# Kernel tuning notes

Measured on AMD Instinct MI355X. Metric: run time of the kernel, lower is better.

## Reference

```python
import jax, jax.numpy as jnp
import numpy as np

DEGREE = 8
HIDDEN = 256
IN_DIM = 3
N_LAYERS = 8  # num_hidden_layers=8 -> 1 input + 6 middle + 1 output ChebyKAN layers


def cheby_layer(x, coeff):
    """x: [P, in], coeff: [in, out, degree+1] -> [P, out].
    Computes tanh(x), Chebyshev recurrence T_0..T_d, and contracts
    sum_d T_d(x)_i * coeff[i, o, d] without materializing the full basis.
    """
    x = jnp.tanh(x)
    t_prev = jnp.ones_like(x)          # T_0
    t_cur = x                          # T_1
    out = jnp.einsum('pi,io->po', t_prev, coeff[:, :, 0])
    out = out + jnp.einsum('pi,io->po', t_cur, coeff[:, :, 1])
    for d in range(2, coeff.shape[-1]):
        t_prev, t_cur = t_cur, 2.0 * x * t_cur - t_prev
        out = out + jnp.einsum('pi,io->po', t_cur, coeff[:, :, d])
    return out


def decode(pts, ws):
    h = pts
    for w in ws:
        h = cheby_layer(h, w)
    return h


def setup_inputs() -> dict:
    key = jax.random.key(0)
    k_nm, k_m, *k_ws = jax.random.split(key, 2 + N_LAYERS)
    B, N = 4, 16384
    inp = {
        'non_mnfld_pnts': jax.random.normal(k_nm, (B, N, IN_DIM), dtype=jnp.float32),
        'mnfld_pnts': jax.random.normal(k_m, (B, N, IN_DIM), dtype=jnp.float32),
    }
    dims = [IN_DIM] + [HIDDEN] * (N_LAYERS - 1) + [1]
    for i in range(N_LAYERS):
        fan_in, fan_out = dims[i], dims[i + 1]
        std = 1.0 / (fan_in * (DEGREE + 1))
        inp[f'w{i}'] = jax.random.normal(k_ws[i], (fan_in, fan_out, DEGREE + 1), dtype=jnp.float32) * std
    return inp


def reference(non_mnfld_pnts, mnfld_pnts, w0, w1, w2, w3, w4, w5, w6, w7):
    ws = [w0, w1, w2, w3, w4, w5, w6, w7]
    B = non_mnfld_pnts.shape[0]
    mnfld_pred = decode(mnfld_pnts.reshape(-1, IN_DIM), ws).reshape(B, -1)
    nonmnfld_pred = decode(non_mnfld_pnts.reshape(-1, IN_DIM), ws).reshape(B, -1)
    return (mnfld_pred, nonmnfld_pred)
```

## Files before the change

### kernel.cpp

```cpp
#include <hip/hip_runtime.h>

typedef _Float16 f16;
typedef __attribute__((ext_vector_type(4)))  _Float16 f16x4;
typedef __attribute__((ext_vector_type(8)))  _Float16 f16x8;
typedef __attribute__((ext_vector_type(16))) float    f32x16;

#define WT_L (8*256*256)

__device__ __forceinline__ float fexp2(float x) {
#if __has_builtin(__builtin_amdgcn_exp2f)
    return __builtin_amdgcn_exp2f(x);
#else
    return exp2f(x);
#endif
}

__device__ __forceinline__ float fast_tanh(float v) {
    float a = __builtin_fabsf(v);
    float e = fexp2(a * -2.8853900817779268f);
    float r = (1.0f - e) * __builtin_amdgcn_rcpf(1.0f + e);
    return __builtin_copysignf(r, v);
}

__global__ void prep_mid(const float* __restrict__ w, f16* __restrict__ wt, float* __restrict__ biasL) {
    __shared__ float red[256];
    const int i = threadIdx.x;
    const int o = blockIdx.x;
    float v[9];
#pragma unroll
    for (int d = 0; d < 9; d++) v[d] = w[(i*256 + o)*9 + d];
#pragma unroll
    for (int d = 1; d < 9; d++) wt[((d-1)*256 + o)*256 + i] = (f16)v[d];
    red[i] = v[0];
    __syncthreads();
#pragma unroll
    for (int s = 128; s > 0; s >>= 1) {
        if (i < s) red[i] += red[i + s];
        __syncthreads();
    }
    if (i == 0) biasL[o] = red[0];
}

__global__ void prep_w0(const float* __restrict__ w0, float* __restrict__ w0t) {
    int id = blockIdx.x*256 + threadIdx.x;
    int i = id / 2304, rem = id % 2304;
    int o = rem / 9, d = rem % 9;
    w0t[(i*9 + d)*256 + o] = w0[id];
}

__global__ void prep_w7(const float* __restrict__ w7, float* __restrict__ w7p) {
    int id = blockIdx.x*256 + threadIdx.x;
    int ch = id / 9, d = id % 9;
    w7p[ch*12 + d] = w7[id];
}

__global__ __launch_bounds__(256, 2)
void kan_mfma(const float* __restrict__ nonm, const float* __restrict__ mnf,
              const f16* __restrict__ wt, const float* __restrict__ bias,
              const float* __restrict__ w0t, const float* __restrict__ w7p,
              float* __restrict__ out)
{
    __shared__ __align__(16) f16 xs[128*256];

    const int t    = threadIdx.x;
    const int b    = blockIdx.x;
    const int lane = t & 63;
    const int w    = t >> 6;
    const int l31  = lane & 31;
    const int half = lane >> 5;
    const int nb   = w * 64;

    const float* src = (b < 512) ? mnf : nonm;
    const int p0 = ((b < 512) ? b : (b - 512)) * 128;

    {
        const int pt = t >> 1;
        const int oh = (t & 1) * 128;
        float c0 = src[(p0 + pt)*3 + 0];
        float c1 = src[(p0 + pt)*3 + 1];
        float c2 = src[(p0 + pt)*3 + 2];
        float xx[3] = {fast_tanh(c0), fast_tanh(c1), fast_tanh(c2)};
        float bas[27];
#pragma unroll
        for (int i = 0; i < 3; i++) {
            float t0 = 1.0f, t1 = xx[i];
            bas[i*9+0] = t0; bas[i*9+1] = t1;
            float x2 = xx[i] + xx[i];
#pragma unroll
            for (int d = 2; d < 9; d++) {
                float t2 = x2*t1 - t0;
                bas[i*9+d] = t2; t0 = t1; t1 = t2;
            }
        }
#pragma unroll 1
        for (int q = 0; q < 32; q++) {
            int o = oh + q*4;
            float4 a = {0.f, 0.f, 0.f, 0.f};
#pragma unroll
            for (int k = 0; k < 27; k++) {
                float4 wv = *(const float4*)(w0t + k*256 + o);
                a.x = fmaf(bas[k], wv.x, a.x);
                a.y = fmaf(bas[k], wv.y, a.y);
                a.z = fmaf(bas[k], wv.z, a.z);
                a.w = fmaf(bas[k], wv.w, a.w);
            }
            f16x4 hv = {(f16)fast_tanh(a.x), (f16)fast_tanh(a.y),
                        (f16)fast_tanh(a.z), (f16)fast_tanh(a.w)};
            int unit = (o >> 3) ^ (pt & 7);
            *(f16x4*)(xs + pt*256 + unit*8 + (o & 7)) = hv;
        }
    }
    __syncthreads();

    f32x16 acc[4][2];
    const f16x8 ones = {(f16)1.f,(f16)1.f,(f16)1.f,(f16)1.f,(f16)1.f,(f16)1.f,(f16)1.f,(f16)1.f};

#pragma unroll 1
    for (int L = 0; L < 6; L++) {
        const f16* wbase = wt + L*WT_L + half*8 + (nb + l31)*256;
        float b0 = bias[L*256 + nb + l31];
        float b1 = bias[L*256 + nb + 32 + l31];
#pragma unroll
        for (int mt = 0; mt < 4; mt++)
#pragma unroll
            for (int r = 0; r < 16; r++) { acc[mt][0][r] = b0; acc[mt][1][r] = b1; }

        f16x8 xv[4], Bb[4][2];
#pragma unroll
        for (int mt = 0; mt < 4; mt++) {
            int m = mt*32 + l31;
            int unit = half ^ (m & 7);
            xv[mt] = *(const f16x8*)(xs + m*256 + unit*8);
        }
#pragma unroll
        for (int j = 0; j < 4; j++) {
            Bb[j][0] = *(const f16x8*)(wbase + j*65536);
            Bb[j][1] = *(const f16x8*)(wbase + j*65536 + 8192);
        }

        f16x8 x2[4], t1[4], t0[4];
#pragma unroll 1
        for (int ck = 0; ck < 16; ck++) {
            const int ckn = (ck < 15) ? ck + 1 : 15;
#pragma unroll
            for (int mt = 0; mt < 4; mt++) {
                t1[mt] = xv[mt];
                x2[mt] = xv[mt] + xv[mt];
                t0[mt] = ones;
            }
#pragma unroll
            for (int mt = 0; mt < 4; mt++) {
                int m = mt*32 + l31;
                int unit = (ckn*2 + half) ^ (m & 7);
                xv[mt] = *(const f16x8*)(xs + m*256 + unit*8);
            }
#pragma unroll
            for (int j = 0; j < 8; j++) {
                const int ck2 = (j < 4) ? ck : ckn;
                const int j2  = (j < 4) ? (j + 4) : (j - 4);
                f16x8 nb0 = *(const f16x8*)(wbase + ck2*16 + j2*65536);
                f16x8 nb1 = *(const f16x8*)(wbase + ck2*16 + j2*65536 + 8192);
#pragma unroll
                for (int mt = 0; mt < 4; mt++) {
                    acc[mt][0] = __builtin_amdgcn_mfma_f32_32x32x16_f16(t1[mt], Bb[j&3][0], acc[mt][0], 0, 0, 0);
                    acc[mt][1] = __builtin_amdgcn_mfma_f32_32x32x16_f16(t1[mt], Bb[j&3][1], acc[mt][1], 0, 0, 0);
                }
                if (j < 7) {
#pragma unroll
                    for (int mt = 0; mt < 4; mt++) {
                        f16x8 tn = x2[mt]*t1[mt] - t0[mt];
                        t0[mt] = t1[mt];
                        t1[mt] = tn;
                    }
                }
                Bb[j&3][0] = nb0;
                Bb[j&3][1] = nb1;
            }
        }
        __syncthreads();
#pragma unroll
        for (int mt = 0; mt < 4; mt++) {
#pragma unroll
            for (int nt = 0; nt < 2; nt++) {
                int ch = nb + nt*32 + l31;
                int cu = ch >> 3, ce = ch & 7;
#pragma unroll
                for (int r = 0; r < 16; r++) {
                    int p = mt*32 + (r & 3) + 8*(r >> 2) + 4*half;
                    int unit = cu ^ (p & 7);
                    xs[p*256 + unit*8 + ce] = (f16)fast_tanh(acc[mt][nt][r]);
                }
            }
        }
        __syncthreads();
    }

    {
        const int pt = t & 127;
        const int hh = t >> 7;
        float s = 0.0f;
#pragma unroll 1
        for (int q = 0; q < 16; q++) {
            int u = hh*16 + q;
            int unit = u ^ (pt & 7);
            f16x8 xv = *(const f16x8*)(xs + pt*256 + unit*8);
#pragma unroll
            for (int e = 0; e < 8; e++) {
                int ch = u*8 + e;
                float x = (float)xv[e];
                const float* wr = w7p + ch*12;
                float4 wa = *(const float4*)(wr);
                float4 wb = *(const float4*)(wr + 4);
                float wc = wr[8];
                float x2 = x + x;
                float t0 = 1.0f, t1v = x;
                s = fmaf(wa.x, t0, s);
                s = fmaf(wa.y, t1v, s);
                float t2 = x2*t1v - t0;  s = fmaf(wa.z, t2, s);
                float t3 = x2*t2 - t1v;  s = fmaf(wa.w, t3, s);
                float t4 = x2*t3 - t2;   s = fmaf(wb.x, t4, s);
                float t5 = x2*t4 - t3;   s = fmaf(wb.y, t5, s);
                float t6 = x2*t5 - t4;   s = fmaf(wb.z, t6, s);
                float t7 = x2*t6 - t5;   s = fmaf(wb.w, t7, s);
                float t8 = x2*t7 - t6;   s = fmaf(wc,  t8, s);
            }
        }
        __syncthreads();
        float* red = (float*)xs;
        red[hh*128 + pt] = s;
        __syncthreads();
        if (t < 128) out[b*128 + t] = red[t] + red[128 + t];
    }
}

extern "C" void kernel_launch(void* const* d_in, const int* in_sizes, int n_in,
                              void* d_out, int out_size, void* d_ws, size_t ws_size,
                              hipStream_t stream) {
    const float* nonm = (const float*)d_in[0];
    const float* mnf  = (const float*)d_in[1];

    char* ws = (char*)d_ws;
    f16*   wtp   = (f16*)ws;
    float* biasp = (float*)(ws + 6*WT_L*2);
    float* w0tp  = (float*)(ws + 6*WT_L*2 + 6*256*4);
    float* w7pp  = (float*)(ws + 6*WT_L*2 + 6*256*4 + 27*256*4);

    for (int L = 0; L < 6; L++)
        prep_mid<<<256, 256, 0, stream>>>((const float*)d_in[3 + L], wtp + L*WT_L, biasp + L*256);
    prep_w0<<<27, 256, 0, stream>>>((const float*)d_in[2], w0tp);
    prep_w7<<<9, 256, 0, stream>>>((const float*)d_in[9], w7pp);

    kan_mfma<<<1024, 256, 0, stream>>>(nonm, mnf, wtp, biasp, w0tp, w7pp, (float*)d_out);
}
```

Baseline: 1.251 ms.

## Split fused KAN kernel into per-layer launches with global activation buffer

The single fused kernel that ran all eight layers per 128-point tile is split into separate kernels: an input-layer kernel, one MFMA kernel launch per middle layer, and an output-layer kernel. Activations round-trip through a global f16 buffer between launches. The first and last layers get their own thread mappings, and the output kernel stages its weights in shared memory. The intent is to improve occupancy and scheduling for the light first and last layers, at the cost of extra global traffic of about 64 MB per layer and several more kernel launches.

```diff
diff --git a/kernel.cpp b/kernel.cpp
--- a/kernel.cpp
+++ b/kernel.cpp
@@ -54,11 +54,51 @@
     w7p[ch*12 + d] = w7[id];
 }
 
+__global__ void k0(const float* __restrict__ nonm, const float* __restrict__ mnf,
+                   const float* __restrict__ w0t, f16* __restrict__ xg) {
+    const int t = threadIdx.x, b = blockIdx.x;
+    const int pt = t & 63;
+    const int oh = (t >> 6) * 64;
+    const int pid = b*64 + pt;
+    const float* src = (pid < 65536) ? mnf : nonm;
+    const int sp = (pid < 65536) ? pid : pid - 65536;
+    float c0 = src[sp*3 + 0];
+    float c1 = src[sp*3 + 1];
+    float c2 = src[sp*3 + 2];
+    float xx[3] = {fast_tanh(c0), fast_tanh(c1), fast_tanh(c2)};
+    float bas[27];
+#pragma unroll
+    for (int i = 0; i < 3; i++) {
+        float t0 = 1.0f, t1 = xx[i];
+        bas[i*9+0] = t0; bas[i*9+1] = t1;
+        float x2 = xx[i] + xx[i];
+#pragma unroll
+        for (int d = 2; d < 9; d++) {
+            float t2 = x2*t1 - t0;
+            bas[i*9+d] = t2; t0 = t1; t1 = t2;
+        }
+    }
+#pragma unroll 1
+    for (int q = 0; q < 16; q++) {
+        int o = oh + q*4;
+        float4 a = {0.f, 0.f, 0.f, 0.f};
+#pragma unroll
+        for (int k = 0; k < 27; k++) {
+            float4 wv = *(const float4*)(w0t + k*256 + o);
+            a.x = fmaf(bas[k], wv.x, a.x);
+            a.y = fmaf(bas[k], wv.y, a.y);
+            a.z = fmaf(bas[k], wv.z, a.z);
+            a.w = fmaf(bas[k], wv.w, a.w);
+        }
+        f16x4 hv = {(f16)fast_tanh(a.x), (f16)fast_tanh(a.y),
+                    (f16)fast_tanh(a.z), (f16)fast_tanh(a.w)};
+        *(f16x4*)(xg + (size_t)pid*256 + o) = hv;
+    }
+}
+
 __global__ __launch_bounds__(256, 2)
-void kan_mfma(const float* __restrict__ nonm, const float* __restrict__ mnf,
-              const f16* __restrict__ wt, const float* __restrict__ bias,
-              const float* __restrict__ w0t, const float* __restrict__ w7p,
-              float* __restrict__ out)
+void k_mid(const f16* __restrict__ wl, const float* __restrict__ biasL,
+           f16* __restrict__ xg)
 {
     __shared__ __align__(16) f16 xs[128*256];
 
@@ -69,168 +109,139 @@
     const int l31  = lane & 31;
     const int half = lane >> 5;
     const int nb   = w * 64;
-
-    const float* src = (b < 512) ? mnf : nonm;
-    const int p0 = ((b < 512) ? b : (b - 512)) * 128;
-
-    {
-        const int pt = t >> 1;
-        const int oh = (t & 1) * 128;
-        float c0 = src[(p0 + pt)*3 + 0];
-        float c1 = src[(p0 + pt)*3 + 1];
-        float c2 = src[(p0 + pt)*3 + 2];
-        float xx[3] = {fast_tanh(c0), fast_tanh(c1), fast_tanh(c2)};
-        float bas[27];
-#pragma unroll
-        for (int i = 0; i < 3; i++) {
-            float t0 = 1.0f, t1 = xx[i];
-            bas[i*9+0] = t0; bas[i*9+1] = t1;
-            float x2 = xx[i] + xx[i];
-#pragma unroll
-            for (int d = 2; d < 9; d++) {
-                float t2 = x2*t1 - t0;
-                bas[i*9+d] = t2; t0 = t1; t1 = t2;
-            }
-        }
-#pragma unroll 1
-        for (int q = 0; q < 32; q++) {
-            int o = oh + q*4;
-            float4 a = {0.f, 0.f, 0.f, 0.f};
-#pragma unroll
-            for (int k = 0; k < 27; k++) {
-                float4 wv = *(const float4*)(w0t + k*256 + o);
-                a.x = fmaf(bas[k], wv.x, a.x);
-                a.y = fmaf(bas[k], wv.y, a.y);
-                a.z = fmaf(bas[k], wv.z, a.z);
-                a.w = fmaf(bas[k], wv.w, a.w);
-            }
-            f16x4 hv = {(f16)fast_tanh(a.x), (f16)fast_tanh(a.y),
-                        (f16)fast_tanh(a.z), (f16)fast_tanh(a.w)};
-            int unit = (o >> 3) ^ (pt & 7);
-            *(f16x4*)(xs + pt*256 + unit*8 + (o & 7)) = hv;
-        }
+    const size_t tile_off = (size_t)b * 128 * 256;
+
+#pragma unroll
+    for (int i = 0; i < 16; i++) {
+        int idx = i*256 + t;
+        int pt = idx >> 5, cu = idx & 31;
+        f16x8 v = *(const f16x8*)(xg + tile_off + (size_t)idx*8);
+        *(f16x8*)(xs + pt*256 + ((cu ^ (pt & 7))*8)) = v;
     }
     __syncthreads();
 
     f32x16 acc[4][2];
     const f16x8 ones = {(f16)1.f,(f16)1.f,(f16)1.f,(f16)1.f,(f16)1.f,(f16)1.f,(f16)1.f,(f16)1.f};
 
+    const f16* wbase = wl + half*8 + (nb + l31)*256;
+    float b0 = biasL[nb + l31];
+    float b1 = biasL[nb + 32 + l31];
+#pragma unroll
+    for (int mt = 0; mt < 4; mt++)
+#pragma unroll
+        for (int r = 0; r < 16; r++) { acc[mt][0][r] = b0; acc[mt][1][r] = b1; }
+
+    f16x8 xv[4], Bb[4][2];
+#pragma unroll
+    for (int mt = 0; mt < 4; mt++) {
+        int m = mt*32 + l31;
+        int unit = half ^ (m & 7);
+        xv[mt] = *(const f16x8*)(xs + m*256 + unit*8);
+    }
+#pragma unroll
+    for (int j = 0; j < 4; j++) {
+        Bb[j][0] = *(const f16x8*)(wbase + j*65536);
+        Bb[j][1] = *(const f16x8*)(wbase + j*65536 + 8192);
+    }
+
+    f16x8 x2[4], t1[4], t0[4];
 #pragma unroll 1
-    for (int L = 0; L < 6; L++) {
-        const f16* wbase = wt + L*WT_L + half*8 + (nb + l31)*256;
-        float b0 = bias[L*256 + nb + l31];
-        float b1 = bias[L*256 + nb + 32 + l31];
-#pragma unroll
-        for (int mt = 0; mt < 4; mt++)
-#pragma unroll
-            for (int r = 0; r < 16; r++) { acc[mt][0][r] = b0; acc[mt][1][r] = b1; }
-
-        f16x8 xv[4], Bb[4][2];
+    for (int ck = 0; ck < 16; ck++) {
+        const int ckn = (ck < 15) ? ck + 1 : 15;
+#pragma unroll
+        for (int mt = 0; mt < 4; mt++) {
+            t1[mt] = xv[mt];
+            x2[mt] = xv[mt] + xv[mt];
+            t0[mt] = ones;
+        }
 #pragma unroll
         for (int mt = 0; mt < 4; mt++) {
             int m = mt*32 + l31;
-            int unit = half ^ (m & 7);
+            int unit = (ckn*2 + half) ^ (m & 7);
             xv[mt] = *(const f16x8*)(xs + m*256 + unit*8);
         }
 #pragma unroll
-        for (int j = 0; j < 4; j++) {
-            Bb[j][0] = *(const f16x8*)(wbase + j*65536);
-            Bb[j][1] = *(const f16x8*)(wbase + j*65536 + 8192);
-        }
-
-        f16x8 x2[4], t1[4], t0[4];
-#pragma unroll 1
-        for (int ck = 0; ck < 16; ck++) {
-            const int ckn = (ck < 15) ? ck + 1 : 15;
+        for (int j = 0; j < 8; j++) {
+            const int ck2 = (j < 4) ? ck : ckn;
+            const int j2  = (j < 4) ? (j + 4) : (j - 4);
+            f16x8 pb0 = *(const f16x8*)(wbase + ck2*16 + j2*65536);
+            f16x8 pb1 = *(const f16x8*)(wbase + ck2*16 + j2*65536 + 8192);
 #pragma unroll
             for (int mt = 0; mt < 4; mt++) {
-                t1[mt] = xv[mt];
-                x2[mt] = xv[mt] + xv[mt];
-                t0[mt] = ones;
+                acc[mt][0] = __builtin_amdgcn_mfma_f32_32x32x16_f16(t1[mt], Bb[j&3][0], acc[mt][0], 0, 0, 0);
+                acc[mt][1] = __builtin_amdgcn_mfma_f32_32x32x16_f16(t1[mt], Bb[j&3][1], acc[mt][1], 0, 0, 0);
             }
-#pragma unroll
-            for (int mt = 0; mt < 4; mt++) {
-                int m = mt*32 + l31;
-                int unit = (ckn*2 + half) ^ (m & 7);
-                xv[mt] = *(const f16x8*)(xs + m*256 + unit*8);
-            }
-#pragma unroll
-            for (int j = 0; j < 8; j++) {
-                const int ck2 = (j < 4) ? ck : ckn;
-                const int j2  = (j < 4) ? (j + 4) : (j - 4);
-                f16x8 nb0 = *(const f16x8*)(wbase + ck2*16 + j2*65536);
-                f16x8 nb1 = *(const f16x8*)(wbase + ck2*16 + j2*65536 + 8192);
+            if (j < 7) {
 #pragma unroll
                 for (int mt = 0; mt < 4; mt++) {
-                    acc[mt][0] = __builtin_amdgcn_mfma_f32_32x32x16_f16(t1[mt], Bb[j&3][0], acc[mt][0], 0, 0, 0);
-                    acc[mt][1] = __builtin_amdgcn_mfma_f32_32x32x16_f16(t1[mt], Bb[j&3][1], acc[mt][1], 0, 0, 0);
-                }
-                if (j < 7) {
-#pragma unroll
-                    for (int mt = 0; mt < 4; mt++) {
-                        f16x8 tn = x2[mt]*t1[mt] - t0[mt];
-                        t0[mt] = t1[mt];
-                        t1[mt] = tn;
-                    }
-                }
-                Bb[j&3][0] = nb0;
-                Bb[j&3][1] = nb1;
-            }
-        }
-        __syncthreads();
-#pragma unroll
-        for (int mt = 0; mt < 4; mt++) {
-#pragma unroll
-            for (int nt = 0; nt < 2; nt++) {
-                int ch = nb + nt*32 + l31;
-                int cu = ch >> 3, ce = ch & 7;
-#pragma unroll
-                for (int r = 0; r < 16; r++) {
-                    int p = mt*32 + (r & 3) + 8*(r >> 2) + 4*half;
-                    int unit = cu ^ (p & 7);
-                    xs[p*256 + unit*8 + ce] = (f16)fast_tanh(acc[mt][nt][r]);
+                    f16x8 tn = x2[mt]*t1[mt] - t0[mt];
+                    t0[mt] = t1[mt];
+                    t1[mt] = tn;
                 }
             }
-        }
-        __syncthreads();
-    }
-
-    {
-        const int pt = t & 127;
-        const int hh = t >> 7;
-        float s = 0.0f;
+            Bb[j&3][0] = pb0;
+            Bb[j&3][1] = pb1;
+        }
+    }
+    __syncthreads();
+
+#pragma unroll
+    for (int mt = 0; mt < 4; mt++) {
+#pragma unroll
+        for (int nt = 0; nt < 2; nt++) {
+            int ch = nb + nt*32 + l31;
+            int cu = ch >> 3, ce = ch & 7;
+#pragma unroll
+            for (int r = 0; r < 16; r++) {
+                int p = mt*32 + (r & 3) + 8*(r >> 2) + 4*half;
+                int unit = cu ^ (p & 7);
+                xs[p*256 + unit*8 + ce] = (f16)fast_tanh(acc[mt][nt][r]);
+            }
+        }
+    }
+    __syncthreads();
+
+#pragma unroll
+    for (int i = 0; i < 16; i++) {
+        int idx = i*256 + t;
+        int pt = idx >> 5, cu = idx & 31;
+        f16x8 v = *(const f16x8*)(xs + pt*256 + ((cu ^ (pt & 7))*8));
+        *(f16x8*)(xg + tile_off + (size_t)idx*8) = v;
+    }
+}
+
+__global__ void k7(const f16* __restrict__ xg, const float* __restrict__ w7p,
+                   float* __restrict__ out) {
+    __shared__ float w7s[256*12];
+    const int t = threadIdx.x, b = blockIdx.x;
+#pragma unroll
+    for (int i = 0; i < 12; i++) w7s[i*256 + t] = w7p[i*256 + t];
+    __syncthreads();
+    const int pid = b*256 + t;
+    const f16* row = xg + (size_t)pid*256;
+    float s = 0.0f;
 #pragma unroll 1
-        for (int q = 0; q < 16; q++) {
-            int u = hh*16 + q;
-            int unit = u ^ (pt & 7);
-            f16x8 xv = *(const f16x8*)(xs + pt*256 + unit*8);
-#pragma unroll
-            for (int e = 0; e < 8; e++) {
-                int ch = u*8 + e;
-                float x = (float)xv[e];
-                const float* wr = w7p + ch*12;
-                float4 wa = *(const float4*)(wr);
-                float4 wb = *(const float4*)(wr + 4);
-                float wc = wr[8];
-                float x2 = x + x;
-                float t0 = 1.0f, t1v = x;
-                s = fmaf(wa.x, t0, s);
-                s = fmaf(wa.y, t1v, s);
-                float t2 = x2*t1v - t0;  s = fmaf(wa.z, t2, s);
-                float t3 = x2*t2 - t1v;  s = fmaf(wa.w, t3, s);
-                float t4 = x2*t3 - t2;   s = fmaf(wb.x, t4, s);
-                float t5 = x2*t4 - t3;   s = fmaf(wb.y, t5, s);
-                float t6 = x2*t5 - t4;   s = fmaf(wb.z, t6, s);
-                float t7 = x2*t6 - t5;   s = fmaf(wb.w, t7, s);
-                float t8 = x2*t7 - t6;   s = fmaf(wc,  t8, s);
-            }
-        }
-        __syncthreads();
-        float* red = (float*)xs;
-        red[hh*128 + pt] = s;
-        __syncthreads();
-        if (t < 128) out[b*128 + t] = red[t] + red[128 + t];
-    }
+    for (int cu = 0; cu < 32; cu++) {
+        f16x8 xv = *(const f16x8*)(row + cu*8);
+#pragma unroll
+        for (int e = 0; e < 8; e++) {
+            int ch = cu*8 + e;
+            const float* wr = w7s + ch*12;
+            float x = (float)xv[e];
+            float x2 = x + x;
+            float t0 = 1.0f, t1v = x;
+            s = fmaf(wr[0], t0, s);
+            s = fmaf(wr[1], t1v, s);
+            float t2 = x2*t1v - t0;  s = fmaf(wr[2], t2, s);
+            float t3 = x2*t2 - t1v;  s = fmaf(wr[3], t3, s);
+            float t4 = x2*t3 - t2;   s = fmaf(wr[4], t4, s);
+            float t5 = x2*t4 - t3;   s = fmaf(wr[5], t5, s);
+            float t6 = x2*t5 - t4;   s = fmaf(wr[6], t6, s);
+            float t7 = x2*t6 - t5;   s = fmaf(wr[7], t7, s);
+            float t8 = x2*t7 - t6;   s = fmaf(wr[8], t8, s);
+        }
+    }
+    out[pid] = s;
 }
 
 extern "C" void kernel_launch(void* const* d_in, const int* in_sizes, int n_in,
@@ -242,13 +253,17 @@
     char* ws = (char*)d_ws;
     f16*   wtp   = (f16*)ws;
     float* biasp = (float*)(ws + 6*WT_L*2);
-    float* w0tp  = (float*)(ws + 6*WT_L*2 + 6*256*4);
-    float* w7pp  = (float*)(ws + 6*WT_L*2 + 6*256*4 + 27*256*4);
+    float* w0tp  = (float*)(ws + 6*WT_L*2 + 6144);
+    float* w7pp  = (float*)(ws + 6*WT_L*2 + 6144 + 27648);
+    f16*   xg    = (f16*)(ws + 6*WT_L*2 + 6144 + 27648 + 12288);
 
     for (int L = 0; L < 6; L++)
         prep_mid<<<256, 256, 0, stream>>>((const float*)d_in[3 + L], wtp + L*WT_L, biasp + L*256);
     prep_w0<<<27, 256, 0, stream>>>((const float*)d_in[2], w0tp);
     prep_w7<<<9, 256, 0, stream>>>((const float*)d_in[9], w7pp);
 
-    kan_mfma<<<1024, 256, 0, stream>>>(nonm, mnf, wtp, biasp, w0tp, w7pp, (float*)d_out);
-}
+    k0<<<2048, 256, 0, stream>>>(nonm, mnf, w0tp, xg);
+    for (int L = 0; L < 6; L++)
+        k_mid<<<1024, 256, 0, stream>>>(wtp + L*WT_L, biasp + L*256, xg);
+    k7<<<512, 256, 0, stream>>>(xg, w7pp, (float*)d_out);
+}
```

Result: no change. 1.233 ms (-1.4%).

## Merge weight prep kernels and split fused MLP into three staged kernels

Applied to the files above, without the earlier changes.

Folds the eight weight-preparation launches into one prep_all kernel. Splits the single persistent kernel into three kernels, each running two layers, that pass activations through a global fp16 scratch buffer. This likely aims to cut launch overhead and to shorten each kernel, perhaps for better scheduling or code generation. In exchange it adds global round-trips for the 128x256 activation tiles and two extra kernel boundaries.

```diff
diff --git a/kernel.cpp b/kernel.cpp
--- a/kernel.cpp
+++ b/kernel.cpp
@@ -22,63 +22,176 @@
     return __builtin_copysignf(r, v);
 }
 
-__global__ void prep_mid(const float* __restrict__ w, f16* __restrict__ wt, float* __restrict__ biasL) {
+__global__ void prep_all(const float* __restrict__ w0, const float* __restrict__ w1,
+                         const float* __restrict__ w2, const float* __restrict__ w3,
+                         const float* __restrict__ w4, const float* __restrict__ w5,
+                         const float* __restrict__ w6, const float* __restrict__ w7,
+                         f16* __restrict__ wt, float* __restrict__ biasp,
+                         float* __restrict__ w0t, float* __restrict__ w7p)
+{
     __shared__ float red[256];
-    const int i = threadIdx.x;
-    const int o = blockIdx.x;
-    float v[9];
-#pragma unroll
-    for (int d = 0; d < 9; d++) v[d] = w[(i*256 + o)*9 + d];
-#pragma unroll
-    for (int d = 1; d < 9; d++) wt[((d-1)*256 + o)*256 + i] = (f16)v[d];
-    red[i] = v[0];
+    const int bi = blockIdx.x, t = threadIdx.x;
+    if (bi < 1536) {
+        const int L = bi >> 8, o = bi & 255, i = t;
+        const float* w;
+        switch (L) { case 0: w = w1; break; case 1: w = w2; break; case 2: w = w3; break;
+                     case 3: w = w4; break; case 4: w = w5; break; default: w = w6; }
+        float v[9];
+#pragma unroll
+        for (int d = 0; d < 9; d++) v[d] = w[(i*256 + o)*9 + d];
+#pragma unroll
+        for (int d = 1; d < 9; d++) wt[L*WT_L + ((d-1)*256 + o)*256 + i] = (f16)v[d];
+        red[i] = v[0];
+        __syncthreads();
+#pragma unroll
+        for (int s = 128; s > 0; s >>= 1) {
+            if (i < s) red[i] += red[i + s];
+            __syncthreads();
+        }
+        if (i == 0) biasp[L*256 + o] = red[0];
+    } else if (bi < 1563) {
+        int id = (bi - 1536)*256 + t;
+        int i = id / 2304, rem = id % 2304;
+        int o = rem / 9, d = rem % 9;
+        w0t[(i*9 + d)*256 + o] = w0[id];
+    } else {
+        int id = (bi - 1563)*256 + t;
+        int ch = id / 9, d = id % 9;
+        w7p[ch*12 + d] = w7[id];
+    }
+}
+
+__device__ __forceinline__ void gemm_layer(f16* __restrict__ xs,
+                                           const f16* __restrict__ wl,
+                                           const float* __restrict__ biasL,
+                                           int l31, int half, int nb)
+{
+    f32x16 acc[4][2];
+    const f16x8 ones = {(f16)1.f,(f16)1.f,(f16)1.f,(f16)1.f,(f16)1.f,(f16)1.f,(f16)1.f,(f16)1.f};
+
+    const f16* wbase = wl + half*8 + (nb + l31)*256;
+    float b0 = biasL[nb + l31];
+    float b1 = biasL[nb + 32 + l31];
+#pragma unroll
+    for (int mt = 0; mt < 4; mt++)
+#pragma unroll
+        for (int r = 0; r < 16; r++) { acc[mt][0][r] = b0; acc[mt][1][r] = b1; }
+
+    f16x8 xv[4], Bb[4][2];
+#pragma unroll
+    for (int mt = 0; mt < 4; mt++) {
+        int m = mt*32 + l31;
+        int unit = half ^ (m & 7);
+        xv[mt] = *(const f16x8*)(xs + m*256 + unit*8);
+    }
+#pragma unroll
+    for (int j = 0; j < 4; j++) {
+        Bb[j][0] = *(const f16x8*)(wbase + j*65536);
+        Bb[j][1] = *(const f16x8*)(wbase + j*65536 + 8192);
+    }
+
+    f16x8 x2[4], t1[4], t0[4];
+#pragma unroll 1
+    for (int ck = 0; ck < 16; ck++) {
+        const int ckn = (ck < 15) ? ck + 1 : 15;
+#pragma unroll
+        for (int mt = 0; mt < 4; mt++) {
+            t1[mt] = xv[mt];
+            x2[mt] = xv[mt] + xv[mt];
+            t0[mt] = ones;
+        }
+#pragma unroll
+        for (int mt = 0; mt < 4; mt++) {
+            int m = mt*32 + l31;
+            int unit = (ckn*2 + half) ^ (m & 7);
+            xv[mt] = *(const f16x8*)(xs + m*256 + unit*8);
+        }
+#pragma unroll
+        for (int j = 0; j < 8; j++) {
+            const int ck2 = (j < 4) ? ck : ckn;
+            const int j2  = (j < 4) ? (j + 4) : (j - 4);
+            f16x8 pb0 = *(const f16x8*)(wbase + ck2*16 + j2*65536);
+            f16x8 pb1 = *(const f16x8*)(wbase + ck2*16 + j2*65536 + 8192);
+#pragma unroll
+            for (int mt = 0; mt < 4; mt++) {
+                acc[mt][0] = __builtin_amdgcn_mfma_f32_32x32x16_f16(t1[mt], Bb[j&3][0], acc[mt][0], 0, 0, 0);
+                acc[mt][1] = __builtin_amdgcn_mfma_f32_32x32x16_f16(t1[mt], Bb[j&3][1], acc[mt][1], 0, 0, 0);
+            }
+            if (j < 7) {
+#pragma unroll
+                for (int mt = 0; mt < 4; mt++) {
+                    f16x8 tn = x2[mt]*t1[mt] - t0[mt];
+                    t0[mt] = t1[mt];
+                    t1[mt] = tn;
+                }
+            }
+            Bb[j&3][0] = pb0;
+            Bb[j&3][1] = pb1;
+        }
+    }
     __syncthreads();
-#pragma unroll
-    for (int s = 128; s > 0; s >>= 1) {
-        if (i < s) red[i] += red[i + s];
-        __syncthreads();
-    }
-    if (i == 0) biasL[o] = red[0];
-}
-
-__global__ void prep_w0(const float* __restrict__ w0, float* __restrict__ w0t) {
-    int id = blockIdx.x*256 + threadIdx.x;
-    int i = id / 2304, rem = id % 2304;
-    int o = rem / 9, d = rem % 9;
-    w0t[(i*9 + d)*256 + o] = w0[id];
-}
-
-__global__ void prep_w7(const float* __restrict__ w7, float* __restrict__ w7p) {
-    int id = blockIdx.x*256 + threadIdx.x;
-    int ch = id / 9, d = id % 9;
-    w7p[ch*12 + d] = w7[id];
+
+#pragma unroll
+    for (int mt = 0; mt < 4; mt++) {
+#pragma unroll
+        for (int nt = 0; nt < 2; nt++) {
+            int ch = nb + nt*32 + l31;
+            int cu = ch >> 3, ce = ch & 7;
+#pragma unroll
+            for (int r = 0; r < 16; r++) {
+                int p = mt*32 + (r & 3) + 8*(r >> 2) + 4*half;
+                int unit = cu ^ (p & 7);
+                xs[p*256 + unit*8 + ce] = (f16)fast_tanh(acc[mt][nt][r]);
+            }
+        }
+    }
+    __syncthreads();
+}
+
+__device__ __forceinline__ void stage_in(f16* __restrict__ xs, const f16* __restrict__ xg,
+                                         size_t tile_off, int t)
+{
+#pragma unroll
+    for (int i = 0; i < 16; i++) {
+        int idx = i*256 + t;
+        int cu = idx >> 7, pt = idx & 127;
+        f16x8 v = *(const f16x8*)(xg + tile_off + (size_t)idx*8);
+        *(f16x8*)(xs + pt*256 + ((cu ^ (pt & 7))*8)) = v;
+    }
+    __syncthreads();
+}
+
+__device__ __forceinline__ void stage_out(const f16* __restrict__ xs, f16* __restrict__ xg,
+                                          size_t tile_off, int t)
+{
+#pragma unroll
+    for (int i = 0; i < 16; i++) {
+        int idx = i*256 + t;
+        int cu = idx >> 7, pt = idx & 127;
+        f16x8 v = *(const f16x8*)(xs + pt*256 + ((cu ^ (pt & 7))*8));
+        *(f16x8*)(xg + tile_off + (size_t)idx*8) = v;
+    }
 }
 
 __global__ __launch_bounds__(256, 2)
-void kan_mfma(const float* __restrict__ nonm, const float* __restrict__ mnf,
-              const f16* __restrict__ wt, const float* __restrict__ bias,
-              const float* __restrict__ w0t, const float* __restrict__ w7p,
-              float* __restrict__ out)
+void kA(const float* __restrict__ nonm, const float* __restrict__ mnf,
+        const float* __restrict__ w0t, const f16* __restrict__ wt,
+        const float* __restrict__ bias, f16* __restrict__ xg)
 {
     __shared__ __align__(16) f16 xs[128*256];
-
-    const int t    = threadIdx.x;
-    const int b    = blockIdx.x;
-    const int lane = t & 63;
-    const int w    = t >> 6;
-    const int l31  = lane & 31;
-    const int half = lane >> 5;
-    const int nb   = w * 64;
-
-    const float* src = (b < 512) ? mnf : nonm;
-    const int p0 = ((b < 512) ? b : (b - 512)) * 128;
+    const int t = threadIdx.x, b = blockIdx.x;
+    const int lane = t & 63, w = t >> 6;
+    const int l31 = lane & 31, half = lane >> 5, nb = w * 64;
 
     {
         const int pt = t >> 1;
         const int oh = (t & 1) * 128;
-        float c0 = src[(p0 + pt)*3 + 0];
-        float c1 = src[(p0 + pt)*3 + 1];
-        float c2 = src[(p0 + pt)*3 + 2];
+        const int pid = b*128 + pt;
+        const float* src = (pid < 65536) ? mnf : nonm;
+        const int sp = (pid < 65536) ? pid : pid - 65536;
+        float c0 = src[sp*3 + 0];
+        float c1 = src[sp*3 + 1];
+        float c2 = src[sp*3 + 2];
         float xx[3] = {fast_tanh(c0), fast_tanh(c1), fast_tanh(c2)};
         float bas[27];
 #pragma unroll
@@ -112,103 +225,55 @@
     }
     __syncthreads();
 
-    f32x16 acc[4][2];
-    const f16x8 ones = {(f16)1.f,(f16)1.f,(f16)1.f,(f16)1.f,(f16)1.f,(f16)1.f,(f16)1.f,(f16)1.f};
-
-#pragma unroll 1
-    for (int L = 0; L < 6; L++) {
-        const f16* wbase = wt + L*WT_L + half*8 + (nb + l31)*256;
-        float b0 = bias[L*256 + nb + l31];
-        float b1 = bias[L*256 + nb + 32 + l31];
-#pragma unroll
-        for (int mt = 0; mt < 4; mt++)
-#pragma unroll
-            for (int r = 0; r < 16; r++) { acc[mt][0][r] = b0; acc[mt][1][r] = b1; }
-
-        f16x8 xv[4], Bb[4][2];
-#pragma unroll
-        for (int mt = 0; mt < 4; mt++) {
-            int m = mt*32 + l31;
-            int unit = half ^ (m & 7);
-            xv[mt] = *(const f16x8*)(xs + m*256 + unit*8);
-        }
-#pragma unroll
-        for (int j = 0; j < 4; j++) {
-            Bb[j][0] = *(const f16x8*)(wbase + j*65536);
-            Bb[j][1] = *(const f16x8*)(wbase + j*65536 + 8192);
-        }
-
-        f16x8 x2[4], t1[4], t0[4];
-#pragma unroll 1
-        for (int ck = 0; ck < 16; ck++) {
-            const int ckn = (ck < 15) ? ck + 1 : 15;
-#pragma unroll
-            for (int mt = 0; mt < 4; mt++) {
-                t1[mt] = xv[mt];
-                x2[mt] = xv[mt] + xv[mt];
-                t0[mt] = ones;
-            }
-#pragma unroll
-            for (int mt = 0; mt < 4; mt++) {
-                int m = mt*32 + l31;
-                int unit = (ckn*2 + half) ^ (m & 7);
-                xv[mt] = *(const f16x8*)(xs + m*256 + unit*8);
-            }
-#pragma unroll
-            for (int j = 0; j < 8; j++) {
-                const int ck2 = (j < 4) ? ck : ckn;
-                const int j2  = (j < 4) ? (j + 4) : (j - 4);
-                f16x8 nb0 = *(const f16x8*)(wbase + ck2*16 + j2*65536);
-                f16x8 nb1 = *(const f16x8*)(wbase + ck2*16 + j2*65536 + 8192);
-#pragma unroll
-                for (int mt = 0; mt < 4; mt++) {
-                    acc[mt][0] = __builtin_amdgcn_mfma_f32_32x32x16_f16(t1[mt], Bb[j&3][0], acc[mt][0], 0, 0, 0);
-                    acc[mt][1] = __builtin_amdgcn_mfma_f32_32x32x16_f16(t1[mt], Bb[j&3][1], acc[mt][1], 0, 0, 0);
-                }
-                if (j < 7) {
-#pragma unroll
-                    for (int mt = 0; mt < 4; mt++) {
-                        f16x8 tn = x2[mt]*t1[mt] - t0[mt];
-                        t0[mt] = t1[mt];
-                        t1[mt] = tn;
-                    }
-                }
-                Bb[j&3][0] = nb0;
-                Bb[j&3][1] = nb1;
-            }
-        }
-        __syncthreads();
-#pragma unroll
-        for (int mt = 0; mt < 4; mt++) {
-#pragma unroll
-            for (int nt = 0; nt < 2; nt++) {
-                int ch = nb + nt*32 + l31;
-                int cu = ch >> 3, ce = ch & 7;
-#pragma unroll
-                for (int r = 0; r < 16; r++) {
-                    int p = mt*32 + (r & 3) + 8*(r >> 2) + 4*half;
-                    int unit = cu ^ (p & 7);
-                    xs[p*256 + unit*8 + ce] = (f16)fast_tanh(acc[mt][nt][r]);
-                }
-            }
-        }
-        __syncthreads();
-    }
+    gemm_layer(xs, wt + 0*WT_L, bias + 0*256, l31, half, nb);
+    gemm_layer(xs, wt + 1*WT_L, bias + 1*256, l31, half, nb);
+
+    stage_out(xs, xg, (size_t)b * 32768, t);
+}
+
+__global__ __launch_bounds__(256, 2)
+void kB(const f16* __restrict__ wt, const float* __restrict__ bias, f16* __restrict__ xg)
+{
+    __shared__ __align__(16) f16 xs[128*256];
+    const int t = threadIdx.x, b = blockIdx.x;
+    const int lane = t & 63, w = t >> 6;
+    const int l31 = lane & 31, half = lane >> 5, nb = w * 64;
+    const size_t tile_off = (size_t)b * 32768;
+
+    stage_in(xs, xg, tile_off, t);
+    gemm_layer(xs, wt + 2*WT_L, bias + 2*256, l31, half, nb);
+    gemm_layer(xs, wt + 3*WT_L, bias + 3*256, l31, half, nb);
+    stage_out(xs, xg, tile_off, t);
+}
+
+__global__ __launch_bounds__(256, 2)
+void kC(const f16* __restrict__ wt, const float* __restrict__ bias,
+        const float* __restrict__ w7p, f16* __restrict__ xg, float* __restrict__ out)
+{
+    __shared__ __align__(16) f16 xs[128*256];
+    const int t = threadIdx.x, b = blockIdx.x;
+    const int lane = t & 63, w = t >> 6;
+    const int l31 = lane & 31, half = lane >> 5, nb = w * 64;
+    const size_t tile_off = (size_t)b * 32768;
+
+    stage_in(xs, xg, tile_off, t);
+    gemm_layer(xs, wt + 4*WT_L, bias + 4*256, l31, half, nb);
+    gemm_layer(xs, wt + 5*WT_L, bias + 5*256, l31, half, nb);
 
     {
         const int pt = t & 127;
-        const int hh = t >> 7;
+        const int seg = t >> 7;
         float s = 0.0f;
 #pragma unroll 1
         for (int q = 0; q < 16; q++) {
-            int u = hh*16 + q;
+            int u = seg*16 + q;
             int unit = u ^ (pt & 7);
             f16x8 xv = *(const f16x8*)(xs + pt*256 + unit*8);
 #pragma unroll
             for (int e = 0; e < 8; e++) {
                 int ch = u*8 + e;
+                const float* wr = w7p + ch*12;
                 float x = (float)xv[e];
-                const float* wr = w7p + ch*12;
                 float4 wa = *(const float4*)(wr);
                 float4 wb = *(const float4*)(wr + 4);
                 float wc = wr[8];
@@ -227,7 +292,7 @@
         }
         __syncthreads();
         float* red = (float*)xs;
-        red[hh*128 + pt] = s;
+        red[seg*128 + pt] = s;
         __syncthreads();
         if (t < 128) out[b*128 + t] = red[t] + red[128 + t];
     }
@@ -242,13 +307,17 @@
     char* ws = (char*)d_ws;
     f16*   wtp   = (f16*)ws;
     float* biasp = (float*)(ws + 6*WT_L*2);
-    float* w0tp  = (float*)(ws + 6*WT_L*2 + 6*256*4);
-    float* w7pp  = (float*)(ws + 6*WT_L*2 + 6*256*4 + 27*256*4);
-
-    for (int L = 0; L < 6; L++)
-        prep_mid<<<256, 256, 0, stream>>>((const float*)d_in[3 + L], wtp + L*WT_L, biasp + L*256);
-    prep_w0<<<27, 256, 0, stream>>>((const float*)d_in[2], w0tp);
-    prep_w7<<<9, 256, 0, stream>>>((const float*)d_in[9], w7pp);
-
-    kan_mfma<<<1024, 256, 0, stream>>>(nonm, mnf, wtp, biasp, w0tp, w7pp, (float*)d_out);
-}
+    float* w0tp  = (float*)(ws + 6*WT_L*2 + 6144);
+    float* w7pp  = (float*)(ws + 6*WT_L*2 + 6144 + 27648);
+    f16*   xg    = (f16*)(ws + 6*WT_L*2 + 6144 + 27648 + 12288);
+
+    prep_all<<<1572, 256, 0, stream>>>((const float*)d_in[2], (const float*)d_in[3],
+                                       (const float*)d_in[4], (const float*)d_in[5],
+                                       (const float*)d_in[6], (const float*)d_in[7],
+                                       (const float*)d_in[8], (const float*)d_in[9],
+                                       wtp, biasp, w0tp, w7pp);
+
+    kA<<<1024, 256, 0, stream>>>(nonm, mnf, w0tp, wtp, biasp, xg);
+    kB<<<1024, 256, 0, stream>>>(wtp, biasp, xg);
+    kC<<<1024, 256, 0, stream>>>(wtp, biasp, w7pp, xg, (float*)d_out);
+}
```

After: 1.318 ms. 1.05x slower.

## Use cooperative grid with per-layer grid syncs and MFMA-friendly weight layout

Applied to the files above, without the earlier changes.

Replaces the 1024-block kernel with a 256-block cooperative kernel of 512 threads, each block handling 256 points per input set, and loops over both point sets in one launch. A grid-wide sync between layers keeps all blocks reading the same layer weights at once, aiming for better L2 reuse. Weights are pre-permuted into a lane-contiguous layout so each wave's B-fragment loads are coalesced. The six prep kernels are merged into one launch. The grid syncs add barrier overhead, and the grid size is tied to the exact input size.

```diff
diff --git a/kernel.cpp b/kernel.cpp
--- a/kernel.cpp
+++ b/kernel.cpp
@@ -1,4 +1,7 @@
 #include <hip/hip_runtime.h>
+#include <hip/hip_cooperative_groups.h>
+
+namespace cg = cooperative_groups;
 
 typedef _Float16 f16;
 typedef __attribute__((ext_vector_type(4)))  _Float16 f16x4;
@@ -22,45 +25,146 @@
     return __builtin_copysignf(r, v);
 }
 
-__global__ void prep_mid(const float* __restrict__ w, f16* __restrict__ wt, float* __restrict__ biasL) {
+__global__ void prep_all(const float* __restrict__ w0, const float* __restrict__ w1,
+                         const float* __restrict__ w2, const float* __restrict__ w3,
+                         const float* __restrict__ w4, const float* __restrict__ w5,
+                         const float* __restrict__ w6, const float* __restrict__ w7,
+                         f16* __restrict__ wt, float* __restrict__ biasp,
+                         float* __restrict__ w0t, float* __restrict__ w7p)
+{
     __shared__ float red[256];
-    const int i = threadIdx.x;
-    const int o = blockIdx.x;
-    float v[9];
-#pragma unroll
-    for (int d = 0; d < 9; d++) v[d] = w[(i*256 + o)*9 + d];
-#pragma unroll
-    for (int d = 1; d < 9; d++) wt[((d-1)*256 + o)*256 + i] = (f16)v[d];
-    red[i] = v[0];
+    const int bi = blockIdx.x, t = threadIdx.x;
+    if (bi < 1536) {
+        const int L = bi >> 8, o = bi & 255, i = t;
+        const float* w;
+        switch (L) { case 0: w = w1; break; case 1: w = w2; break; case 2: w = w3; break;
+                     case 3: w = w4; break; case 4: w = w5; break; default: w = w6; }
+        float v[9];
+#pragma unroll
+        for (int d = 0; d < 9; d++) v[d] = w[(i*256 + o)*9 + d];
+        const int ck = i >> 4, k = i & 15;
+        const int nsl = o >> 6, nt = (o >> 5) & 1, l31 = o & 31;
+        const int lane = (k >> 3)*32 + l31, e = k & 7;
+        const int base = ck*4096 + nsl*1024 + nt*512 + lane*8 + e;
+#pragma unroll
+        for (int d = 1; d < 9; d++)
+            wt[L*WT_L + (d-1)*16*4096 + base] = (f16)v[d];
+        red[i] = v[0];
+        __syncthreads();
+#pragma unroll
+        for (int s = 128; s > 0; s >>= 1) {
+            if (i < s) red[i] += red[i + s];
+            __syncthreads();
+        }
+        if (i == 0) biasp[L*256 + o] = red[0];
+    } else if (bi < 1563) {
+        int id = (bi - 1536)*256 + t;
+        int i = id / 2304, rem = id % 2304;
+        int o = rem / 9, d = rem % 9;
+        w0t[(i*9 + d)*256 + o] = w0[id];
+    } else {
+        int id = (bi - 1563)*256 + t;
+        int ch = id / 9, d = id % 9;
+        w7p[ch*12 + d] = w7[id];
+    }
+}
+
+__device__ __forceinline__ void gemm_layer(f16* __restrict__ xs,
+                                           const f16* __restrict__ wbase,
+                                           const float* __restrict__ biasL,
+                                           int l31, int half, int nb, int mh)
+{
+    f32x16 acc[4][2];
+    const f16x8 ones = {(f16)1.f,(f16)1.f,(f16)1.f,(f16)1.f,(f16)1.f,(f16)1.f,(f16)1.f,(f16)1.f};
+    const int mrow = mh * 128;
+
+    float b0 = biasL[nb + l31];
+    float b1 = biasL[nb + 32 + l31];
+#pragma unroll
+    for (int mt = 0; mt < 4; mt++)
+#pragma unroll
+        for (int r = 0; r < 16; r++) { acc[mt][0][r] = b0; acc[mt][1][r] = b1; }
+
+    f16x8 xv[4], Bb[4][2];
+#pragma unroll
+    for (int mt = 0; mt < 4; mt++) {
+        int m = mrow + mt*32 + l31;
+        int unit = half ^ (m & 7);
+        xv[mt] = *(const f16x8*)(xs + m*256 + unit*8);
+    }
+#pragma unroll
+    for (int j = 0; j < 4; j++) {
+        Bb[j][0] = *(const f16x8*)(wbase + j*16*4096);
+        Bb[j][1] = *(const f16x8*)(wbase + j*16*4096 + 512);
+    }
+
+    f16x8 x2[4], t1[4], t0v[4];
+#pragma unroll 1
+    for (int ck = 0; ck < 16; ck++) {
+        const int ckn = (ck < 15) ? ck + 1 : 15;
+#pragma unroll
+        for (int mt = 0; mt < 4; mt++) {
+            t1[mt]  = xv[mt];
+            x2[mt]  = xv[mt] + xv[mt];
+            t0v[mt] = ones;
+        }
+#pragma unroll
+        for (int mt = 0; mt < 4; mt++) {
+            int m = mrow + mt*32 + l31;
+            int unit = (ckn*2 + half) ^ (m & 7);
+            xv[mt] = *(const f16x8*)(xs + m*256 + unit*8);
+        }
+#pragma unroll
+        for (int j = 0; j < 8; j++) {
+            const int ck2 = (j < 4) ? ck : ckn;
+            const int j2  = (j < 4) ? (j + 4) : (j - 4);
+            const int off = (j2*16 + ck2)*4096;
+            f16x8 pb0 = *(const f16x8*)(wbase + off);
+            f16x8 pb1 = *(const f16x8*)(wbase + off + 512);
+#pragma unroll
+            for (int mt = 0; mt < 4; mt++) {
+                acc[mt][0] = __builtin_amdgcn_mfma_f32_32x32x16_f16(t1[mt], Bb[j&3][0], acc[mt][0], 0, 0, 0);
+                acc[mt][1] = __builtin_amdgcn_mfma_f32_32x32x16_f16(t1[mt], Bb[j&3][1], acc[mt][1], 0, 0, 0);
+            }
+            if (j < 7) {
+#pragma unroll
+                for (int mt = 0; mt < 4; mt++) {
+                    f16x8 tn = x2[mt]*t1[mt] - t0v[mt];
+                    t0v[mt] = t1[mt];
+                    t1[mt]  = tn;
+                }
+            }
+            Bb[j&3][0] = pb0;
+            Bb[j&3][1] = pb1;
+        }
+    }
     __syncthreads();
-#pragma unroll
-    for (int s = 128; s > 0; s >>= 1) {
-        if (i < s) red[i] += red[i + s];
-        __syncthreads();
-    }
-    if (i == 0) biasL[o] = red[0];
-}
-
-__global__ void prep_w0(const float* __restrict__ w0, float* __restrict__ w0t) {
-    int id = blockIdx.x*256 + threadIdx.x;
-    int i = id / 2304, rem = id % 2304;
-    int o = rem / 9, d = rem % 9;
-    w0t[(i*9 + d)*256 + o] = w0[id];
-}
-
-__global__ void prep_w7(const float* __restrict__ w7, float* __restrict__ w7p) {
-    int id = blockIdx.x*256 + threadIdx.x;
-    int ch = id / 9, d = id % 9;
-    w7p[ch*12 + d] = w7[id];
-}
-
-__global__ __launch_bounds__(256, 2)
-void kan_mfma(const float* __restrict__ nonm, const float* __restrict__ mnf,
+
+#pragma unroll
+    for (int mt = 0; mt < 4; mt++) {
+#pragma unroll
+        for (int nt = 0; nt < 2; nt++) {
+            int ch = nb + nt*32 + l31;
+            int cu = ch >> 3, ce = ch & 7;
+#pragma unroll
+            for (int r = 0; r < 16; r++) {
+                int p = mrow + mt*32 + (r & 3) + 8*(r >> 2) + 4*half;
+                int unit = cu ^ (p & 7);
+                xs[p*256 + unit*8 + ce] = (f16)fast_tanh(acc[mt][nt][r]);
+            }
+        }
+    }
+    __syncthreads();
+}
+
+__global__ __launch_bounds__(512, 2)
+void kan_coop(const float* __restrict__ nonm, const float* __restrict__ mnf,
               const f16* __restrict__ wt, const float* __restrict__ bias,
               const float* __restrict__ w0t, const float* __restrict__ w7p,
               float* __restrict__ out)
 {
-    __shared__ __align__(16) f16 xs[128*256];
+    __shared__ __align__(16) f16 xs[256*256];
+    cg::grid_group grid = cg::this_grid();
 
     const int t    = threadIdx.x;
     const int b    = blockIdx.x;
@@ -68,168 +172,101 @@
     const int w    = t >> 6;
     const int l31  = lane & 31;
     const int half = lane >> 5;
-    const int nb   = w * 64;
-
-    const float* src = (b < 512) ? mnf : nonm;
-    const int p0 = ((b < 512) ? b : (b - 512)) * 128;
-
-    {
-        const int pt = t >> 1;
-        const int oh = (t & 1) * 128;
-        float c0 = src[(p0 + pt)*3 + 0];
-        float c1 = src[(p0 + pt)*3 + 1];
-        float c2 = src[(p0 + pt)*3 + 2];
-        float xx[3] = {fast_tanh(c0), fast_tanh(c1), fast_tanh(c2)};
-        float bas[27];
-#pragma unroll
-        for (int i = 0; i < 3; i++) {
-            float t0 = 1.0f, t1 = xx[i];
-            bas[i*9+0] = t0; bas[i*9+1] = t1;
-            float x2 = xx[i] + xx[i];
-#pragma unroll
-            for (int d = 2; d < 9; d++) {
-                float t2 = x2*t1 - t0;
-                bas[i*9+d] = t2; t0 = t1; t1 = t2;
-            }
-        }
-#pragma unroll 1
-        for (int q = 0; q < 32; q++) {
-            int o = oh + q*4;
-            float4 a = {0.f, 0.f, 0.f, 0.f};
-#pragma unroll
-            for (int k = 0; k < 27; k++) {
-                float4 wv = *(const float4*)(w0t + k*256 + o);
-                a.x = fmaf(bas[k], wv.x, a.x);
-                a.y = fmaf(bas[k], wv.y, a.y);
-                a.z = fmaf(bas[k], wv.z, a.z);
-                a.w = fmaf(bas[k], wv.w, a.w);
-            }
-            f16x4 hv = {(f16)fast_tanh(a.x), (f16)fast_tanh(a.y),
-                        (f16)fast_tanh(a.z), (f16)fast_tanh(a.w)};
-            int unit = (o >> 3) ^ (pt & 7);
-            *(f16x4*)(xs + pt*256 + unit*8 + (o & 7)) = hv;
-        }
-    }
-    __syncthreads();
-
-    f32x16 acc[4][2];
-    const f16x8 ones = {(f16)1.f,(f16)1.f,(f16)1.f,(f16)1.f,(f16)1.f,(f16)1.f,(f16)1.f,(f16)1.f};
-
-#pragma unroll 1
-    for (int L = 0; L < 6; L++) {
-        const f16* wbase = wt + L*WT_L + half*8 + (nb + l31)*256;
-        float b0 = bias[L*256 + nb + l31];
-        float b1 = bias[L*256 + nb + 32 + l31];
-#pragma unroll
-        for (int mt = 0; mt < 4; mt++)
-#pragma unroll
-            for (int r = 0; r < 16; r++) { acc[mt][0][r] = b0; acc[mt][1][r] = b1; }
-
-        f16x8 xv[4], Bb[4][2];
-#pragma unroll
-        for (int mt = 0; mt < 4; mt++) {
-            int m = mt*32 + l31;
-            int unit = half ^ (m & 7);
-            xv[mt] = *(const f16x8*)(xs + m*256 + unit*8);
-        }
-#pragma unroll
-        for (int j = 0; j < 4; j++) {
-            Bb[j][0] = *(const f16x8*)(wbase + j*65536);
-            Bb[j][1] = *(const f16x8*)(wbase + j*65536 + 8192);
-        }
-
-        f16x8 x2[4], t1[4], t0[4];
-#pragma unroll 1
-        for (int ck = 0; ck < 16; ck++) {
-            const int ckn = (ck < 15) ? ck + 1 : 15;
-#pragma unroll
-            for (int mt = 0; mt < 4; mt++) {
-                t1[mt] = xv[mt];
-                x2[mt] = xv[mt] + xv[mt];
-                t0[mt] = ones;
-            }
-#pragma unroll
-            for (int mt = 0; mt < 4; mt++) {
-                int m = mt*32 + l31;
-                int unit = (ckn*2 + half) ^ (m & 7);
-                xv[mt] = *(const f16x8*)(xs + m*256 + unit*8);
-            }
-#pragma unroll
-            for (int j = 0; j < 8; j++) {
-                const int ck2 = (j < 4) ? ck : ckn;
-                const int j2  = (j < 4) ? (j + 4) : (j - 4);
-                f16x8 nb0 = *(const f16x8*)(wbase + ck2*16 + j2*65536);
-                f16x8 nb1 = *(const f16x8*)(wbase + ck2*16 + j2*65536 + 8192);
-#pragma unroll
-                for (int mt = 0; mt < 4; mt++) {
-                    acc[mt][0] = __builtin_amdgcn_mfma_f32_32x32x16_f16(t1[mt], Bb[j&3][0], acc[mt][0], 0, 0, 0);
-                    acc[mt][1] = __builtin_amdgcn_mfma_f32_32x32x16_f16(t1[mt], Bb[j&3][1], acc[mt][1], 0, 0, 0);
-                }
-                if (j < 7) {
-#pragma unroll
-                    for (int mt = 0; mt < 4; mt++) {
-                        f16x8 tn = x2[mt]*t1[mt] - t0[mt];
-                        t0[mt] = t1[mt];
-                        t1[mt] = tn;
-                    }
-                }
-                Bb[j&3][0] = nb0;
-                Bb[j&3][1] = nb1;
+    const int mh   = w >> 2;
+    const int nsl  = w & 3;
+    const int nb   = nsl * 64;
+
+#pragma unroll 1
+    for (int h = 0; h < 2; h++) {
+        const float* src = h ? nonm : mnf;
+
+        {
+            const int pt = t >> 1;
+            const int oh = (t & 1) * 128;
+            const int pid = b*256 + pt;
+            float c0 = src[pid*3 + 0];
+            float c1 = src[pid*3 + 1];
+            float c2 = src[pid*3 + 2];
+            float xx[3] = {fast_tanh(c0), fast_tanh(c1), fast_tanh(c2)};
+            float bas[27];
+#pragma unroll
+            for (int i = 0; i < 3; i++) {
+                float t0 = 1.0f, t1 = xx[i];
+                bas[i*9+0] = t0; bas[i*9+1] = t1;
+                float x2 = xx[i] + xx[i];
+#pragma unroll
+                for (int d = 2; d < 9; d++) {
+                    float t2 = x2*t1 - t0;
+                    bas[i*9+d] = t2; t0 = t1; t1 = t2;
+                }
+            }
+#pragma unroll 1
+            for (int q = 0; q < 32; q++) {
+                int o = oh + q*4;
+                float4 a = {0.f, 0.f, 0.f, 0.f};
+#pragma unroll
+                for (int k = 0; k < 27; k++) {
+                    float4 wv = *(const float4*)(w0t + k*256 + o);
+                    a.x = fmaf(bas[k], wv.x, a.x);
+                    a.y = fmaf(bas[k], wv.y, a.y);
+                    a.z = fmaf(bas[k], wv.z, a.z);
+                    a.w = fmaf(bas[k], wv.w, a.w);
+                }
+                f16x4 hv = {(f16)fast_tanh(a.x), (f16)fast_tanh(a.y),
+                            (f16)fast_tanh(a.z), (f16)fast_tanh(a.w)};
+                int unit = (o >> 3) ^ (pt & 7);
+                *(f16x4*)(xs + pt*256 + unit*8 + (o & 7)) = hv;
             }
         }
         __syncthreads();
-#pragma unroll
-        for (int mt = 0; mt < 4; mt++) {
-#pragma unroll
-            for (int nt = 0; nt < 2; nt++) {
-                int ch = nb + nt*32 + l31;
-                int cu = ch >> 3, ce = ch & 7;
-#pragma unroll
-                for (int r = 0; r < 16; r++) {
-                    int p = mt*32 + (r & 3) + 8*(r >> 2) + 4*half;
-                    int unit = cu ^ (p & 7);
-                    xs[p*256 + unit*8 + ce] = (f16)fast_tanh(acc[mt][nt][r]);
-                }
-            }
-        }
-        __syncthreads();
-    }
-
-    {
-        const int pt = t & 127;
-        const int hh = t >> 7;
-        float s = 0.0f;
-#pragma unroll 1
-        for (int q = 0; q < 16; q++) {
-            int u = hh*16 + q;
-            int unit = u ^ (pt & 7);
-            f16x8 xv = *(const f16x8*)(xs + pt*256 + unit*8);
-#pragma unroll
-            for (int e = 0; e < 8; e++) {
-                int ch = u*8 + e;
-                float x = (float)xv[e];
-                const float* wr = w7p + ch*12;
-                float4 wa = *(const float4*)(wr);
-                float4 wb = *(const float4*)(wr + 4);
-                float wc = wr[8];
-                float x2 = x + x;
-                float t0 = 1.0f, t1v = x;
-                s = fmaf(wa.x, t0, s);
-                s = fmaf(wa.y, t1v, s);
-                float t2 = x2*t1v - t0;  s = fmaf(wa.z, t2, s);
-                float t3 = x2*t2 - t1v;  s = fmaf(wa.w, t3, s);
-                float t4 = x2*t3 - t2;   s = fmaf(wb.x, t4, s);
-                float t5 = x2*t4 - t3;   s = fmaf(wb.y, t5, s);
-                float t6 = x2*t5 - t4;   s = fmaf(wb.z, t6, s);
-                float t7 = x2*t6 - t5;   s = fmaf(wb.w, t7, s);
-                float t8 = x2*t7 - t6;   s = fmaf(wc,  t8, s);
-            }
-        }
-        __syncthreads();
-        float* red = (float*)xs;
-        red[hh*128 + pt] = s;
-        __syncthreads();
-        if (t < 128) out[b*128 + t] = red[t] + red[128 + t];
+
+#pragma unroll 1
+        for (int L = 0; L < 6; L++) {
+            if (L) grid.sync();
+            const f16* wbase = wt + L*WT_L + nsl*1024 + lane*8;
+            gemm_layer(xs, wbase, bias + L*256, l31, half, nb, mh);
+        }
+
+        {
+            const int pt = t & 255;
+            const int seg = t >> 8;
+            float s = 0.0f;
+#pragma unroll 1
+            for (int q = 0; q < 16; q++) {
+                int u = seg*16 + q;
+                int unit = u ^ (pt & 7);
+                f16x8 xv = *(const f16x8*)(xs + pt*256 + unit*8);
+#pragma unroll
+                for (int e = 0; e < 8; e++) {
+                    int ch = u*8 + e;
+                    const float* wr = w7p + ch*12;
+                    float x = (float)xv[e];
+                    float4 wa = *(const float4*)(wr);
+                    float4 wb = *(const float4*)(wr + 4);
+                    float wc = wr[8];
+                    float x2 = x + x;
+                    float t0 = 1.0f, t1v = x;
+                    s = fmaf(wa.x, t0, s);
+                    s = fmaf(wa.y, t1v, s);
+                    float t2 = x2*t1v - t0;  s = fmaf(wa.z, t2, s);
+                    float t3 = x2*t2 - t1v;  s = fmaf(wa.w, t3, s);
+                    float t4 = x2*t3 - t2;   s = fmaf(wb.x, t4, s);
+                    float t5 = x2*t4 - t3;   s = fmaf(wb.y, t5, s);
+                    float t6 = x2*t5 - t4;   s = fmaf(wb.z, t6, s);
+                    float t7 = x2*t6 - t5;   s = fmaf(wb.w, t7, s);
+                    float t8 = x2*t7 - t6;   s = fmaf(wc,  t8, s);
+                }
+            }
+            __syncthreads();
+            float* red = (float*)xs;
+            red[seg*256 + pt] = s;
+            __syncthreads();
+            if (t < 256) out[h*65536 + b*256 + t] = red[t] + red[256 + t];
+        }
+        if (h == 0) {
+            __syncthreads();
+            grid.sync();
+        }
     }
 }
 
@@ -242,13 +279,17 @@
     char* ws = (char*)d_ws;
     f16*   wtp   = (f16*)ws;
     float* biasp = (float*)(ws + 6*WT_L*2);
-    float* w0tp  = (float*)(ws + 6*WT_L*2 + 6*256*4);
-    float* w7pp  = (float*)(ws + 6*WT_L*2 + 6*256*4 + 27*256*4);
-
-    for (int L = 0; L < 6; L++)
-        prep_mid<<<256, 256, 0, stream>>>((const float*)d_in[3 + L], wtp + L*WT_L, biasp + L*256);
-    prep_w0<<<27, 256, 0, stream>>>((const float*)d_in[2], w0tp);
-    prep_w7<<<9, 256, 0, stream>>>((const float*)d_in[9], w7pp);
-
-    kan_mfma<<<1024, 256, 0, stream>>>(nonm, mnf, wtp, biasp, w0tp, w7pp, (float*)d_out);
-}
+    float* w0tp  = (float*)(ws + 6*WT_L*2 + 6144);
+    float* w7pp  = (float*)(ws + 6*WT_L*2 + 6144 + 27648);
+
+    prep_all<<<1572, 256, 0, stream>>>((const float*)d_in[2], (const float*)d_in[3],
+                                       (const float*)d_in[4], (const float*)d_in[5],
+                                       (const float*)d_in[6], (const float*)d_in[7],
+                                       (const float*)d_in[8], (const float*)d_in[9],
+                                       wtp, biasp, w0tp, w7pp);
+
+    float* outp = (float*)d_out;
+    void* args[] = {(void*)&nonm, (void*)&mnf, (void*)&wtp, (void*)&biasp,
+                    (void*)&w0tp, (void*)&w7pp, (void*)&outp};
+    hipLaunchCooperativeKernel((void*)kan_coop, dim3(256), dim3(512), args, 0, stream);
+}
```

New measurement: 1.440 ms. +15.1%, slower.
